# Kernel tuning notes

Hardware: AMD Instinct MI355X
Metric: run time of the kernel (lower is better)

## Reference

```python
import jax, jax.numpy as jnp
import numpy as np

N_ATOMS = 1_000_000
DESC_DIM = 128
HIDDEN = 128
N_ELEM = 4  # element ids 0..3


def setup_inputs() -> dict:
    key = jax.random.key(0)
    ks = jax.random.split(key, 6)
    element = jax.random.randint(ks[0], (N_ATOMS,), 0, N_ELEM, dtype=jnp.int32)
    desc = jax.random.normal(ks[1], (N_ATOMS, DESC_DIM), dtype=jnp.float32)
    # Per-element MLP experts: desc_dim -> hidden -> 1
    W1 = jax.random.normal(ks[2], (N_ELEM, DESC_DIM, HIDDEN), dtype=jnp.float32) / np.sqrt(DESC_DIM)
    b1 = jnp.zeros((N_ELEM, HIDDEN), dtype=jnp.float32)
    W2 = jax.random.normal(ks[3], (N_ELEM, HIDDEN), dtype=jnp.float32) / np.sqrt(HIDDEN)
    b2 = jnp.zeros((N_ELEM,), dtype=jnp.float32)
    return {"element": element, "desc": desc, "W1": W1, "b1": b1, "W2": W2, "b2": b2}


def reference(element, desc, W1, b1, W2, b2):
    """Per-element dispatch: each atom's descriptor goes through the MLP for
    its atomic number. JAX jit needs static shapes, so we compute each
    expert densely and select with where (loop over small fixed expert set)."""
    out = jnp.zeros(desc.shape[0], dtype=desc.dtype)
    for e in range(W1.shape[0]):
        h = jax.nn.relu(desc @ W1[e] + b1[e])      # [N, HIDDEN]
        y = h @ W2[e] + b2[e]                       # [N]
        out = jnp.where(element == e, y, out)
    return out
```

## Files before the change

kernel.cpp:

```cpp
#include <hip/hip_runtime.h>
#include <hip/hip_bf16.h>

typedef __attribute__((ext_vector_type(8))) short short8;
typedef __attribute__((ext_vector_type(4))) float float4v;

__device__ __forceinline__ unsigned short f2bf(float f) {
    unsigned int u = __float_as_uint(f);
    u += 0x7fffu + ((u >> 16) & 1u);
    return (unsigned short)(u >> 16);
}

__global__ void count_kernel(const int* __restrict__ elem, int n, int* __restrict__ bc) {
    const int t = threadIdx.x, b = blockIdx.x;
    const int base = b * 1024;
    int c[4] = {0, 0, 0, 0};
    #pragma unroll
    for (int i = 0; i < 4; ++i) {
        const int a = base + i * 256 + t;
        if (a < n) c[elem[a]]++;
    }
    int p0 = c[0] | (c[1] << 16);
    int p1 = c[2] | (c[3] << 16);
    #pragma unroll
    for (int off = 1; off < 64; off <<= 1) { p0 += __shfl_xor(p0, off); p1 += __shfl_xor(p1, off); }
    __shared__ int wsum[4][4];
    const int w = t >> 6, lane = t & 63;
    if (lane == 0) {
        wsum[w][0] = p0 & 0xffff; wsum[w][1] = p0 >> 16;
        wsum[w][2] = p1 & 0xffff; wsum[w][3] = p1 >> 16;
    }
    __syncthreads();
    if (t < 4) {
        int s = 0;
        #pragma unroll
        for (int ww = 0; ww < 4; ++ww) s += wsum[ww][t];
        bc[b * 4 + t] = s;
    }
}

__global__ void scan_kernel(int* __restrict__ bc, int* __restrict__ offs, int nb) {
    const int t = threadIdx.x, w = t >> 6, lane = t & 63;
    int vals[16];
    int s = 0;
    #pragma unroll
    for (int j = 0; j < 16; ++j) {
        const int i = lane * 16 + j;
        const int v = (i < nb) ? bc[i * 4 + w] : 0;
        vals[j] = s; s += v;
    }
    int incl = s;
    #pragma unroll
    for (int off = 1; off < 64; off <<= 1) {
        const int v = __shfl_up(incl, off);
        if (lane >= off) incl += v;
    }
    const int excl = incl - s;
    __shared__ int tot[4];
    __shared__ int eoff[4];
    if (lane == 63) tot[w] = incl;
    __syncthreads();
    if (t == 0) {
        int a = 0;
        for (int e = 0; e < 4; ++e) { eoff[e] = a; offs[e] = a; a += tot[e]; }
        offs[4] = a;
    }
    __syncthreads();
    const int myoff = eoff[w] + excl;
    #pragma unroll
    for (int j = 0; j < 16; ++j) {
        const int i = lane * 16 + j;
        if (i < nb) bc[i * 4 + w] = myoff + vals[j];
    }
}

__global__ void scatter_kernel(const int* __restrict__ elem, int n,
                               const int* __restrict__ bc, int* __restrict__ idx_sorted) {
    const int t = threadIdx.x, b = blockIdx.x;
    const int w = t >> 6, lane = t & 63;
    const int base = b * 1024;
    int ev[4];
    #pragma unroll
    for (int i = 0; i < 4; ++i) {
        const int a = base + i * 256 + t;
        ev[i] = (a < n) ? elem[a] : -1;
    }
    __shared__ int tbl[4][4][4];
    __shared__ int sbase[4];
    #pragma unroll
    for (int i = 0; i < 4; ++i) {
        #pragma unroll
        for (int el = 0; el < 4; ++el) {
            const unsigned long long m = __ballot(ev[i] == el);
            if (lane == 0) tbl[i][w][el] = (int)__popcll(m);
        }
    }
    if (t < 4) sbase[t] = bc[b * 4 + t];
    __syncthreads();
    if (t < 4) {
        int s = 0;
        for (int i = 0; i < 4; ++i)
            for (int w2 = 0; w2 < 4; ++w2) { const int v = tbl[i][w2][t]; tbl[i][w2][t] = s; s += v; }
    }
    __syncthreads();
    #pragma unroll
    for (int i = 0; i < 4; ++i) {
        unsigned long long m[4];
        #pragma unroll
        for (int el = 0; el < 4; ++el) m[el] = __ballot(ev[i] == el);
        const int a = base + i * 256 + t;
        if (a < n) {
            const int el = ev[i];
            const int rank = (int)__popcll(m[el] & ((1ull << lane) - 1ull));
            idx_sorted[sbase[el] + tbl[i][w][el] + rank] = a;
        }
    }
}

__global__ void w1t_kernel(const float* __restrict__ W1, unsigned short* __restrict__ W1T) {
    const int b = blockIdx.x;
    const int e = b >> 7, nn = b & 127;
    const int k = threadIdx.x;
    const float v = W1[((size_t)(e * 128 + k)) * 128 + nn];
    W1T[((size_t)(e * 128 + nn)) * 128 + k] = f2bf(v);
}

__global__ __launch_bounds__(256, 2)
void expert_mlp_kernel(const float* __restrict__ desc,
                       const unsigned short* __restrict__ W1T,
                       const float* __restrict__ b1,
                       const float* __restrict__ W2,
                       const float* __restrict__ b2,
                       const int* __restrict__ idx_sorted,
                       const int* __restrict__ offs,
                       float* __restrict__ out) {
    __shared__ unsigned short As[128 * 128];
    __shared__ unsigned short Bs[128 * 128];

    const int bx = blockIdx.x;
    const int e = bx & 3;
    const int tile = bx >> 2;
    const int base = offs[e];
    const int cnt = offs[e + 1] - base;
    const int m0 = tile * 128;
    if (m0 >= cnt) return;
    const int t = threadIdx.x;

    {
        const uint4* src = (const uint4*)(W1T + (size_t)e * 16384);
        const int c = t & 15, nrow = t >> 4;
        #pragma unroll
        for (int p = 0; p < 8; ++p) {
            const int nn = nrow + p * 16;
            const uint4 v = src[nn * 16 + c];
            const int pc = c ^ (nn & 7);
            *(uint4*)(&Bs[nn * 128 + pc * 8]) = v;
        }
    }
    {
        const int c = t & 31, rr = t >> 5;
        #pragma unroll
        for (int p = 0; p < 16; ++p) {
            const int r = p * 8 + rr;
            const int gm = m0 + r;
            const int gi = idx_sorted[base + ((gm < cnt) ? gm : 0)];
            const float4 v = *(const float4*)(desc + (size_t)gi * 128 + c * 4);
            ushort4 pk;
            pk.x = f2bf(v.x); pk.y = f2bf(v.y); pk.z = f2bf(v.z); pk.w = f2bf(v.w);
            const int pc = (c >> 1) ^ (r & 7);
            *(ushort4*)(&As[r * 128 + pc * 8 + (c & 1) * 4]) = pk;
        }
    }
    __syncthreads();

    const int lane = t & 63;
    const int wv = t >> 6;
    const int quad = lane >> 4;
    const int l16 = lane & 15;
    const int mbase = wv * 32;
    const int r7 = l16 & 7;

    float4v acc[2][8] = {};
    #pragma unroll
    for (int ks = 0; ks < 4; ++ks) {
        const int pco = ((ks * 4 + quad) ^ r7) * 8;
        const short8 a0 = *(const short8*)(&As[(mbase + l16) * 128 + pco]);
        const short8 a1 = *(const short8*)(&As[(mbase + 16 + l16) * 128 + pco]);
        #pragma unroll
        for (int nt = 0; nt < 8; ++nt) {
            const short8 bf = *(const short8*)(&Bs[(nt * 16 + l16) * 128 + pco]);
            acc[0][nt] = __builtin_amdgcn_mfma_f32_16x16x32_bf16(a0, bf, acc[0][nt], 0, 0, 0);
            acc[1][nt] = __builtin_amdgcn_mfma_f32_16x16x32_bf16(a1, bf, acc[1][nt], 0, 0, 0);
        }
    }

    float b1v[8], w2v[8];
    #pragma unroll
    for (int nt = 0; nt < 8; ++nt) {
        b1v[nt] = b1[e * 128 + nt * 16 + l16];
        w2v[nt] = W2[e * 128 + nt * 16 + l16];
    }
    const float b2e = b2[e];
    #pragma unroll
    for (int mt = 0; mt < 2; ++mt) {
        float y[4] = {0.f, 0.f, 0.f, 0.f};
        #pragma unroll
        for (int nt = 0; nt < 8; ++nt) {
            const float4v v = acc[mt][nt];
            #pragma unroll
            for (int r = 0; r < 4; ++r)
                y[r] += fmaxf(v[r] + b1v[nt], 0.f) * w2v[nt];
        }
        #pragma unroll
        for (int off = 1; off < 16; off <<= 1) {
            #pragma unroll
            for (int r = 0; r < 4; ++r) y[r] += __shfl_xor(y[r], off, 16);
        }
        if (l16 == 0) {
            #pragma unroll
            for (int r = 0; r < 4; ++r) {
                const int m = mbase + mt * 16 + quad * 4 + r;
                const int gm = m0 + m;
                if (gm < cnt) out[idx_sorted[base + gm]] = y[r] + b2e;
            }
        }
    }
}

extern "C" void kernel_launch(void* const* d_in, const int* in_sizes, int n_in,
                              void* d_out, int out_size, void* d_ws, size_t ws_size,
                              hipStream_t stream) {
    const int*   elem = (const int*)d_in[0];
    const float* desc = (const float*)d_in[1];
    const float* W1   = (const float*)d_in[2];
    const float* b1   = (const float*)d_in[3];
    const float* W2   = (const float*)d_in[4];
    const float* b2   = (const float*)d_in[5];
    float* out = (float*)d_out;
    const int n = in_sizes[0];

    char* ws = (char*)d_ws;
    int* bc         = (int*)ws;
    int* offs       = (int*)(ws + 16128);
    int* idx_sorted = (int*)(ws + 16384);
    unsigned short* W1T = (unsigned short*)(ws + 16384 + (size_t)n * 4);

    const int nb = (n + 1023) / 1024;
    count_kernel  <<<nb, 256, 0, stream>>>(elem, n, bc);
    scan_kernel   <<<1, 256, 0, stream>>>(bc, offs, nb);
    scatter_kernel<<<nb, 256, 0, stream>>>(elem, n, bc, idx_sorted);
    w1t_kernel    <<<512, 128, 0, stream>>>(W1, W1T);

    const int tiles = (n + 127) / 128;
    expert_mlp_kernel<<<tiles * 4, 256, 0, stream>>>(desc, W1T, b1, W2, b2, idx_sorted, offs, out);
}
```

Baseline: 692.2 us.

## Fuse W1 transpose into count kernel, read B from global, compact tile grid

Merges the W1 transpose/bf16 conversion into the count kernel as extra blocks, which removes one launch. The expert MLP kernel now loads W1T fragments directly from global memory (L2-resident) instead of staging them in LDS. This halves shared memory per block, so launch bounds are raised to 4 blocks per CU. The grid is also compacted so tiles map to experts by prefix counts, removing the roughly 4x early-exit blocks. The trade-off is extra global/L2 traffic for B fragments and a non-unrolled k-loop.

```diff
diff --git a/kernel.cpp b/kernel.cpp
--- a/kernel.cpp
+++ b/kernel.cpp
@@ -10,8 +10,19 @@
     return (unsigned short)(u >> 16);
 }
 
-__global__ void count_kernel(const int* __restrict__ elem, int n, int* __restrict__ bc) {
-    const int t = threadIdx.x, b = blockIdx.x;
+__global__ void count_w1t_kernel(const int* __restrict__ elem, int n, int* __restrict__ bc,
+                                 const float* __restrict__ W1, unsigned short* __restrict__ W1T,
+                                 int nb) {
+    const int b = blockIdx.x;
+    const int t = threadIdx.x;
+    if (b >= nb) {
+        const int local = b - nb;
+        const int p = local * 2 + (t >> 7);
+        const int e = p >> 7, nn = p & 127, k = t & 127;
+        const float v = W1[((size_t)(e * 128 + k)) * 128 + nn];
+        W1T[((size_t)(e * 128 + nn)) * 128 + k] = f2bf(v);
+        return;
+    }
     const int base = b * 1024;
     int c[4] = {0, 0, 0, 0};
     #pragma unroll
@@ -116,15 +127,7 @@
     }
 }
 
-__global__ void w1t_kernel(const float* __restrict__ W1, unsigned short* __restrict__ W1T) {
-    const int b = blockIdx.x;
-    const int e = b >> 7, nn = b & 127;
-    const int k = threadIdx.x;
-    const float v = W1[((size_t)(e * 128 + k)) * 128 + nn];
-    W1T[((size_t)(e * 128 + nn)) * 128 + k] = f2bf(v);
-}
-
-__global__ __launch_bounds__(256, 2)
+__global__ __launch_bounds__(256, 4)
 void expert_mlp_kernel(const float* __restrict__ desc,
                        const unsigned short* __restrict__ W1T,
                        const float* __restrict__ b1,
@@ -134,28 +137,29 @@
                        const int* __restrict__ offs,
                        float* __restrict__ out) {
     __shared__ unsigned short As[128 * 128];
-    __shared__ unsigned short Bs[128 * 128];
-
-    const int bx = blockIdx.x;
-    const int e = bx & 3;
-    const int tile = bx >> 2;
-    const int base = offs[e];
-    const int cnt = offs[e + 1] - base;
+
+    const int o0 = offs[0], o1 = offs[1], o2 = offs[2], o3 = offs[3], o4 = offs[4];
+    const int c0 = o1 - o0, c1 = o2 - o1, c2 = o3 - o2, c3 = o4 - o3;
+    const int t0 = (c0 + 127) >> 7, t1 = (c1 + 127) >> 7, t2 = (c2 + 127) >> 7, t3 = (c3 + 127) >> 7;
+    int tile = blockIdx.x;
+    int e, base, cnt;
+    if (tile < t0) { e = 0; base = o0; cnt = c0; }
+    else {
+        tile -= t0;
+        if (tile < t1) { e = 1; base = o1; cnt = c1; }
+        else {
+            tile -= t1;
+            if (tile < t2) { e = 2; base = o2; cnt = c2; }
+            else {
+                tile -= t2;
+                if (tile >= t3) return;
+                e = 3; base = o3; cnt = c3;
+            }
+        }
+    }
     const int m0 = tile * 128;
-    if (m0 >= cnt) return;
     const int t = threadIdx.x;
 
-    {
-        const uint4* src = (const uint4*)(W1T + (size_t)e * 16384);
-        const int c = t & 15, nrow = t >> 4;
-        #pragma unroll
-        for (int p = 0; p < 8; ++p) {
-            const int nn = nrow + p * 16;
-            const uint4 v = src[nn * 16 + c];
-            const int pc = c ^ (nn & 7);
-            *(uint4*)(&Bs[nn * 128 + pc * 8]) = v;
-        }
-    }
     {
         const int c = t & 31, rr = t >> 5;
         #pragma unroll
@@ -179,17 +183,22 @@
     const int mbase = wv * 32;
     const int r7 = l16 & 7;
 
+    const unsigned short* Bp = W1T + (size_t)e * 16384 + (size_t)l16 * 128 + quad * 8;
+
     float4v acc[2][8] = {};
-    #pragma unroll
+    #pragma unroll 1
     for (int ks = 0; ks < 4; ++ks) {
         const int pco = ((ks * 4 + quad) ^ r7) * 8;
         const short8 a0 = *(const short8*)(&As[(mbase + l16) * 128 + pco]);
         const short8 a1 = *(const short8*)(&As[(mbase + 16 + l16) * 128 + pco]);
+        short8 bfr[8];
+        #pragma unroll
+        for (int nt = 0; nt < 8; ++nt)
+            bfr[nt] = *(const short8*)(Bp + ks * 32 + nt * 2048);
         #pragma unroll
         for (int nt = 0; nt < 8; ++nt) {
-            const short8 bf = *(const short8*)(&Bs[(nt * 16 + l16) * 128 + pco]);
-            acc[0][nt] = __builtin_amdgcn_mfma_f32_16x16x32_bf16(a0, bf, acc[0][nt], 0, 0, 0);
-            acc[1][nt] = __builtin_amdgcn_mfma_f32_16x16x32_bf16(a1, bf, acc[1][nt], 0, 0, 0);
+            acc[0][nt] = __builtin_amdgcn_mfma_f32_16x16x32_bf16(a0, bfr[nt], acc[0][nt], 0, 0, 0);
+            acc[1][nt] = __builtin_amdgcn_mfma_f32_16x16x32_bf16(a1, bfr[nt], acc[1][nt], 0, 0, 0);
         }
     }
 
@@ -242,14 +251,14 @@
     int* bc         = (int*)ws;
     int* offs       = (int*)(ws + 16128);
     int* idx_sorted = (int*)(ws + 16384);
-    unsigned short* W1T = (unsigned short*)(ws + 16384 + (size_t)n * 4);
+    const size_t idx_bytes = ((size_t)n * 4 + 255) & ~(size_t)255;
+    unsigned short* W1T = (unsigned short*)(ws + 16384 + idx_bytes);
 
     const int nb = (n + 1023) / 1024;
-    count_kernel  <<<nb, 256, 0, stream>>>(elem, n, bc);
-    scan_kernel   <<<1, 256, 0, stream>>>(bc, offs, nb);
-    scatter_kernel<<<nb, 256, 0, stream>>>(elem, n, bc, idx_sorted);
-    w1t_kernel    <<<512, 128, 0, stream>>>(W1, W1T);
-
-    const int tiles = (n + 127) / 128;
-    expert_mlp_kernel<<<tiles * 4, 256, 0, stream>>>(desc, W1T, b1, W2, b2, idx_sorted, offs, out);
-}
+    count_w1t_kernel<<<nb + 256, 256, 0, stream>>>(elem, n, bc, W1, W1T, nb);
+    scan_kernel     <<<1, 256, 0, stream>>>(bc, offs, nb);
+    scatter_kernel  <<<nb, 256, 0, stream>>>(elem, n, bc, idx_sorted);
+
+    const int tiles_up = (n >> 7) + 8;
+    expert_mlp_kernel<<<tiles_up, 256, 0, stream>>>(desc, W1T, b1, W2, b2, idx_sorted, offs, out);
+}
```

Result: slower. 760.6 us (+9.9%).
